# Kernel tuning notes

Hardware: AMD Instinct MI355X
Metric: run time of the kernel (lower is better)

## Reference

```python
import jax, jax.numpy as jnp
import numpy as np

FIR_LO = {
    'db4': np.array([-0.0105974017850021, 0.0328830116668852, 0.0308413818355607, -0.1870348117188811,
                     -0.0279837694169839, 0.6308807679295904, 0.7148465705529155, 0.2303778133088964], np.float32),
    'db6': np.array([0.00107730108499558, -0.00477725751101065, -0.0005538422009938, 0.03158203931748603,
                     0.02752286553030533, -0.0975016055873225, -0.12976686756709563, 0.22626469396544,
                     0.3152503517092432, -0.7511339080210959, 0.4946238903984534, 0.1115407433501095], np.float32),
    'sym6': np.array([-0.007800708325034148, 0.001767711864242804, 0.04472490177066578, -0.02106029251230056,
                      -0.0726375227866, 0.3379294217282401, 0.787641141030194, 0.4910559419267466,
                      -0.048311742585632, -0.1179901111484105, 0.00349071208421747, 0.01540410932702737], np.float32),
    'coif5': np.array([-3.459977283621256e-05, -7.098330313814114e-05, 0.0004662169601128863, 0.001117518770890601,
                       -0.002574517688750223, -0.00900797613666158, 0.015880544863615904, 0.03455502757306163,
                       -0.08230192710688598, -0.07179982161931202, 0.42848347637761874, 0.7937772226256206,
                       0.4051769024096169, -0.06112339000267287, -0.06577191128185562, 0.023452696141836267,
                       0.007782596427325418, -0.003793512864491014, -0.0002606761356811993, 0.000107502882505652,
                       1.10319778524429e-05, -5.520763127949e-06, -1.0682196848076e-06, 5.236425333584e-07,
                       1.125098976034e-07, -5.417490769329e-08, -8.8631e-09, 4.2921e-09, 6.7e-10, -3.2e-10], np.float32),
}

CANDIDATES = ['db4', 'db6', 'sym6', 'coif5', 'bior53', 'bior97']
LIFT_53 = [(-0.5, True), (0.25, False)]
LIFT_97 = [(-1.586134342, True), (-0.05298011854, False), (0.8829110762, True), (0.4435068522, False)]


def _pad_reflect(x, hpad, wpad):
    if hpad == (0, 0) and wpad == (0, 0):
        return x
    return jnp.pad(x, ((0, 0), (0, 0), hpad, wpad), mode='reflect')


def _lo(name):
    lo = jnp.asarray(FIR_LO[name])
    return lo / (jnp.sqrt(jnp.sum(lo * lo)) + 1e-12)


def _hi_from_lo(lo):
    L = lo.shape[0]
    sign = jnp.cos(jnp.pi * jnp.arange(L, dtype=lo.dtype))  # (-1)^n
    return sign * lo[::-1]


def _sep_conv(x, k, dim):
    # x: (N,1,H,W); k: (L,) 1D filter applied separably along dim (cross-correlation, stride 1)
    L = k.shape[0]
    pl = (L - 1) // 2
    pa, pb = ((pl - 1, pl) if L % 2 == 0 else (pl, pl))
    if dim == 'W':
        xp = _pad_reflect(x, (0, 0), (pa, pb))
        kern = k.reshape(1, 1, 1, L)
    else:
        xp = _pad_reflect(x, (pa, pb), (0, 0))
        kern = k.reshape(1, 1, L, 1)
    return jax.lax.conv_general_dilated(xp, kern, (1, 1), 'VALID',
                                        dimension_numbers=('NCHW', 'OIHW', 'NCHW'))


def _split_even_odd(x, dim):
    if dim == 'W':
        if x.shape[3] % 2 == 1:
            x = _pad_reflect(x, (0, 0), (0, 1))
        return x[..., 0::2], x[..., 1::2]
    if x.shape[2] % 2 == 1:
        x = _pad_reflect(x, (0, 1), (0, 0))
    return x[..., 0::2, :], x[..., 1::2, :]


def _nb_sum(x, dim):
    # 0.5*(left+right) with reflect padding == conv with kernel [0.5, 0, 0.5]
    if dim == 'W':
        xp = _pad_reflect(x, (0, 0), (1, 1))
        return 0.5 * (xp[..., :-2] + xp[..., 2:])
    xp = _pad_reflect(x, (1, 1), (0, 0))
    return 0.5 * (xp[..., :-2, :] + xp[..., 2:, :])


def _lift(x, dim, steps, sA, sD):
    even, odd = _split_even_odd(x, dim)
    for coeff, is_pred in steps:
        if is_pred:
            odd = odd + coeff * _nb_sum(even, dim)
        else:
            even = even + coeff * _nb_sum(odd, dim)
    return sA * even, sD * odd


def _one_level_1d(x, cand, dim, p):
    if cand == 'bior53':
        return _lift(x, dim, LIFT_53, p['s53A'], p['s53D'])
    if cand == 'bior97':
        return _lift(x, dim, LIFT_97, p['s97A'], p['s97D'])
    lo = _lo(cand)
    return _sep_conv(x, lo, dim), _sep_conv(x, _hi_from_lo(lo), dim)


def _one_level_2d(x, cand, p):
    H, W = x.shape[2], x.shape[3]
    Lw, Hw = _one_level_1d(x, cand, 'W', p)
    LL, LH = _one_level_1d(Lw, cand, 'H', p)
    HL, HH = _one_level_1d(Hw, cand, 'H', p)

    def up(t):
        if t.shape[2] == H and t.shape[3] == W:
            return t
        return jax.image.resize(t, (t.shape[0], t.shape[1], H, W), method='bilinear')  # align_corners=False

    hf = p['hf']
    return up(LL), up(LH) * hf, up(HL) * hf, up(HH) * hf


def reference(x, gate_w1, gate_b1, gate_w2, gate_b2, scale53_A, scale53_D,
              scale97_A, scale97_D, hf_scale, proj_w, proj_b):
    B, C, H, W = x.shape
    # gate: 1x1 conv -> relu -> 1x1 conv -> softmax over K candidates
    h = jax.nn.relu(jnp.einsum('bchw,oc->bohw', x, gate_w1) + gate_b1[None, :, None, None])
    logits = jnp.einsum('bchw,oc->bohw', h, gate_w2) + gate_b2[None, :, None, None]
    gate_w = jax.nn.softmax(logits, axis=1)  # (B,K,H,W)

    x_bc = x.reshape(B * C, 1, H, W)
    p = {'s53A': scale53_A, 's53D': scale53_D, 's97A': scale97_A, 's97D': scale97_D, 'hf': hf_scale}
    bands = [_one_level_2d(x_bc, c, p) for c in CANDIDATES]
    # stack over K candidates -> (B*C, K, H, W) per subband
    LL = jnp.concatenate([b[0] for b in bands], axis=1)
    LH = jnp.concatenate([b[1] for b in bands], axis=1)
    HL = jnp.concatenate([b[2] for b in bands], axis=1)
    HH = jnp.concatenate([b[3] for b in bands], axis=1)

    w = jnp.repeat(gate_w, C, axis=0)  # (B*C,K,H,W), same as repeat_interleave on batch
    w = w / (jnp.sum(w, axis=1, keepdims=True) + 1e-12)
    LL_f = jnp.sum(LL * w, axis=1)
    LH_f = jnp.sum(LH * w, axis=1)
    HL_f = jnp.sum(HL * w, axis=1)
    HH_f = jnp.sum(HH * w, axis=1)

    Y = jnp.stack([LL_f, LH_f, HL_f, HH_f], axis=1).reshape(B, C * 4, H, W)
    return jnp.einsum('bchw,oc->bohw', Y, proj_w) + proj_b[None, :, None, None]


def setup_inputs() -> dict:
    key = jax.random.key(0)
    ks = jax.random.split(key, 5)
    C, hidden, K, Cout = 32, 8, 6, 32
    return {
        'x': jax.random.normal(ks[0], (4, C, 192, 192), jnp.float32),
        'gate_w1': jax.random.normal(ks[1], (hidden, C), jnp.float32) * (1.0 / np.sqrt(C)),
        'gate_b1': jnp.zeros((hidden,), jnp.float32),
        'gate_w2': jax.random.normal(ks[2], (K, hidden), jnp.float32) * (1.0 / np.sqrt(hidden)),
        'gate_b2': jnp.zeros((K,), jnp.float32),
        'scale53_A': jnp.float32(1.0),
        'scale53_D': jnp.float32(1.0),
        'scale97_A': jnp.float32(1.149604398),
        'scale97_D': jnp.float32(1.0 / 1.149604398),
        'hf_scale': jnp.float32(0.9),
        'proj_w': jax.random.normal(ks[3], (Cout, 4 * C), jnp.float32) * (1.0 / np.sqrt(4 * C)),
        'proj_b': jnp.zeros((Cout,), jnp.float32),
    }
```

## Files before the change

kernel.cpp:

```cpp
#include <hip/hip_runtime.h>
#include <hip/hip_fp16.h>

#define HW 36864
#define IMGS 128

typedef _Float16 h16;
typedef _Float16 v8h __attribute__((ext_vector_type(8)));
typedef _Float16 v4h __attribute__((ext_vector_type(4)));
typedef _Float16 v2h __attribute__((ext_vector_type(2)));
typedef float v4f __attribute__((ext_vector_type(4)));

static __device__ __forceinline__ int imax(int a, int b) { return a > b ? a : b; }
static __device__ __forceinline__ int imin(int a, int b) { return a < b ? a : b; }

__device__ __constant__ float LIFT_C[6] = {
  -0.5f, 0.25f,
  -1.586134342f, -0.05298011854f, 0.8829110762f, 0.4435068522f
};
__device__ __constant__ int FIR_L[4]   = {8, 12, 12, 30};
__device__ __constant__ int FIR_PA[4]  = {2, 4, 4, 13};
__device__ __constant__ int FIR_OFF[4] = {0, 8, 20, 32};

__device__ constexpr float FIRC[62] = {
  -0.0105974017850021f, 0.0328830116668852f, 0.0308413818355607f, -0.1870348117188811f,
  -0.0279837694169839f, 0.6308807679295904f, 0.7148465705529155f, 0.2303778133088964f,
  0.00107730108499558f, -0.00477725751101065f, -0.0005538422009938f, 0.03158203931748603f,
  0.02752286553030533f, -0.0975016055873225f, -0.12976686756709563f, 0.22626469396544f,
  0.3152503517092432f, -0.7511339080210959f, 0.4946238903984534f, 0.1115407433501095f,
  -0.007800708325034148f, 0.001767711864242804f, 0.04472490177066578f, -0.02106029251230056f,
  -0.0726375227866f, 0.3379294217282401f, 0.787641141030194f, 0.4910559419267466f,
  -0.048311742585632f, -0.1179901111484105f, 0.00349071208421747f, 0.01540410932702737f,
  -3.459977283621256e-05f, -7.098330313814114e-05f, 0.0004662169601128863f, 0.001117518770890601f,
  -0.002574517688750223f, -0.00900797613666158f, 0.015880544863615904f, 0.03455502757306163f,
  -0.08230192710688598f, -0.07179982161931202f, 0.42848347637761874f, 0.7937772226256206f,
  0.4051769024096169f, -0.06112339000267287f, -0.06577191128185562f, 0.023452696141836267f,
  0.007782596427325418f, -0.003793512864491014f, -0.0002606761356811993f, 0.000107502882505652f,
  1.10319778524429e-05f, -5.520763127949e-06f, -1.0682196848076e-06f, 5.236425333584e-07f,
  1.125098976034e-07f, -5.417490769329e-08f, -8.8631e-09f, 4.2921e-09f, 6.7e-10f, -3.2e-10f,
};

__global__ __launch_bounds__(256) void k_gate(
    const float* __restrict__ x, const float* __restrict__ w1, const float* __restrict__ b1,
    const float* __restrict__ w2, const float* __restrict__ b2, h16* __restrict__ gate,
    h16* __restrict__ x16)
{
  __shared__ float w1s[256], b1s[8], w2s[48], b2s[6];
  int tid = threadIdx.x;
  w1s[tid] = w1[tid];
  if (tid < 8)  b1s[tid] = b1[tid];
  if (tid < 48) w2s[tid] = w2[tid];
  if (tid < 6)  b2s[tid] = b2[tid];
  __syncthreads();
  int px = blockIdx.x * 256 + tid;
  int b = px / HW, p = px - b * HW;
  const float* xb = x + (size_t)b * 32 * HW + p;
  h16* x16b = x16 + (size_t)b * 32 * HW + p;
  float xv[32];
#pragma unroll
  for (int c = 0; c < 32; ++c) xv[c] = xb[(size_t)c * HW];
#pragma unroll
  for (int c = 0; c < 32; ++c) x16b[(size_t)c * HW] = (h16)xv[c];
  float hb[8];
#pragma unroll
  for (int j = 0; j < 8; ++j) {
    float s = b1s[j];
#pragma unroll
    for (int c = 0; c < 32; ++c) s += w1s[j * 32 + c] * xv[c];
    hb[j] = fmaxf(s, 0.f);
  }
  float e[6], mx = -1e30f;
#pragma unroll
  for (int k = 0; k < 6; ++k) {
    float s = b2s[k];
#pragma unroll
    for (int j = 0; j < 8; ++j) s += w2s[k * 8 + j] * hb[j];
    e[k] = s; mx = fmaxf(mx, s);
  }
  float se = 0.f;
#pragma unroll
  for (int k = 0; k < 6; ++k) { e[k] = expf(e[k] - mx); se += e[k]; }
  float inv = 1.f / se, s2 = 0.f;
#pragma unroll
  for (int k = 0; k < 6; ++k) { e[k] *= inv; s2 += e[k]; }
  float inv2 = 1.f / (s2 + 1e-12f);
  h16* gp = gate + (size_t)b * 6 * HW + p;
#pragma unroll
  for (int k = 0; k < 6; ++k) gp[(size_t)k * HW] = (h16)(e[k] * inv2);
}

__global__ __launch_bounds__(64) void k_build(
    h16* __restrict__ Kall, const float* __restrict__ s53A, const float* __restrict__ s53D,
    const float* __restrict__ s97A, const float* __restrict__ s97D)
{
  const int col = blockIdx.x;
  const int mat = blockIdx.y;
  const int cand = mat >> 1, side = mat & 1;
  const int tid = threadIdx.x;
  h16* out = Kall + (size_t)mat * HW;
  if (cand < 4) {
    const int Lf = FIR_L[cand], PA = FIR_PA[cand], OFF = FIR_OFF[cand];
    float ss = 0.f;
    for (int j = 0; j < Lf; ++j) ss += FIRC[OFF + j] * FIRC[OFF + j];
    const float invn = 1.f / (sqrtf(ss) + 1e-12f);
    for (int i = tid; i < 192; i += 64) {
      const int d = (i < 96) ? 1 : 2;
      const int q0 = i - d;
      const int i0 = imax(q0, 0), i1 = imin(q0 + 1, 189);
      const float tt = (float)d - (float)(2 * i + 1) * (1.f / 192.f);
      float c0 = 0.f, c1 = 0.f;
      for (int j = 0; j < Lf; ++j) {
        float fj = side ? (((j & 1) ? -1.f : 1.f) * FIRC[OFF + Lf - 1 - j]) : FIRC[OFF + j];
        fj *= invn;
        int r0 = i0 + j - PA; r0 = r0 < 0 ? -r0 : (r0 > 191 ? 382 - r0 : r0);
        int r1 = i1 + j - PA; r1 = r1 < 0 ? -r1 : (r1 > 191 ? 382 - r1 : r1);
        if (r0 == col) c0 += fj;
        if (r1 == col) c1 += fj;
      }
      out[(size_t)i * 192 + col] = (h16)((1.f - tt) * c0 + tt * c1);
    }
  } else {
    __shared__ float yb[192];
    __shared__ float sb[96];
    yb[tid] = 0.f; yb[tid + 64] = 0.f; yb[tid + 128] = 0.f;
    __syncthreads();
    if (tid == 0) yb[col] = 1.f;
    __syncthreads();
    const int c97 = (cand == 5);
    const int base = c97 ? 2 : 0, ns = c97 ? 4 : 2;
    for (int s = 0; s < ns; ++s) {
      const float cf = LIFT_C[base + s] * 0.5f;
      for (int j = tid; j < 96; j += 64) {
        int jm = (j == 0) ? 1 : j - 1, jp = (j == 95) ? 94 : j + 1;
        if ((s & 1) == 0) yb[2 * j + 1] += cf * (yb[2 * jm] + yb[2 * jp]);
        else              yb[2 * j]     += cf * (yb[2 * jm + 1] + yb[2 * jp + 1]);
      }
      __syncthreads();
    }
    const float sA = c97 ? s97A[0] : s53A[0];
    const float sD = c97 ? s97D[0] : s53D[0];
    for (int u = tid; u < 96; u += 64)
      sb[u] = side ? sD * yb[2 * u + 1] : sA * yb[2 * u];
    __syncthreads();
    for (int i = tid; i < 192; i += 64) {
      const int u0 = (i >> 1) + (i & 1) - 1;
      const float tt = (i & 1) ? 0.25f : 0.75f;
      const int a0 = imax(u0, 0), a1 = imin(u0 + 1, 95);
      out[(size_t)i * 192 + col] = (h16)((1.f - tt) * sb[a0] + tt * sb[a1]);
    }
  }
}

__global__ __launch_bounds__(512, 2) void k_fuse(
    const h16* __restrict__ Kall, const h16* __restrict__ x16, const h16* __restrict__ gate,
    const float* __restrict__ hfp, h16* __restrict__ sf)
{
  __shared__ h16 Xs[192 * 136];
  __shared__ h16 Bs[48 * 200];
  const int bx = blockIdx.x;
  const int sw = bx & 1, qt = bx >> 1;
  const int img = blockIdx.y;
  const int bimg = img >> 5;
  const int tid = threadIdx.x;
  const int lane = tid & 63, wv = tid >> 6;
  const int lm = lane & 15, quad = lane >> 4;
  const int sh = wv & 1, w4 = wv >> 1;
  const int w0q = qt * 48;
  int ktb = (w0q - 24) >> 5; ktb = ktb < 0 ? 0 : (ktb > 2 ? 2 : ktb);

  const h16* xi = x16 + (size_t)img * HW + ktb * 32;
  for (int u = tid; u < 3072; u += 512) {
    int r = u >> 4, c8 = u & 15;
    *(v8h*)(Xs + r * 136 + c8 * 8) = *(const v8h*)(xi + (size_t)r * 192 + c8 * 8);
  }

  v4f acc[3][3];
#pragma unroll
  for (int mi = 0; mi < 3; ++mi)
#pragma unroll
    for (int nt = 0; nt < 3; ++nt) acc[mi][nt] = (v4f){0.f, 0.f, 0.f, 0.f};

  __syncthreads();

  for (int cand = 0; cand < 6; ++cand) {
    const h16* KW = Kall + (size_t)(cand * 2 + sw) * HW;
    for (int t = wv; t < 36; t += 8) {
      const int mi2 = t % 3, hj = t / 3;
      const int m0w = w0q + mi2 * 16;
      const int n0h = hj * 16;
      int ktr = (m0w - 24) >> 5; ktr = ktr < 0 ? 0 : (ktr > 3 ? 3 : ktr);
      v4f C = (v4f){0.f, 0.f, 0.f, 0.f};
#pragma unroll
      for (int kt = 0; kt < 3; ++kt) {
        const int s = ktr + kt;
        v8h aK = *(const v8h*)(KW + (size_t)(m0w + lm) * 192 + s * 32 + quad * 8);
        v8h bX = *(const v8h*)(Xs + (size_t)(n0h + lm) * 136 + (s - ktb) * 32 + quad * 8);
        C = __builtin_amdgcn_mfma_f32_16x16x32_f16(aK, bX, C, 0, 0, 0);
      }
#pragma unroll
      for (int r = 0; r < 4; ++r)
        Bs[(size_t)(mi2 * 16 + quad * 4 + r) * 200 + n0h + lm] = (h16)C[r];
    }
    __syncthreads();
    const h16* g16 = gate + (size_t)(bimg * 6 + cand) * HW;
    const h16* KB = Kall + (size_t)(cand * 2 + sh) * HW;
#pragma unroll
    for (int mi = 0; mi < 3; ++mi) {
      const int m0 = w4 * 48 + mi * 16;
      const int ktlo = imax(0, (m0 - 24) >> 5), kthi = imin(5, (m0 + 39) >> 5);
      const int hr0 = m0 + quad * 4;
      float g[3][4];
#pragma unroll
      for (int nt = 0; nt < 3; ++nt)
#pragma unroll
        for (int r = 0; r < 4; ++r)
          g[nt][r] = (float)g16[(size_t)(hr0 + r) * 192 + w0q + nt * 16 + lm];
      v4f C[3];
#pragma unroll
      for (int nt = 0; nt < 3; ++nt) C[nt] = (v4f){0.f, 0.f, 0.f, 0.f};
      for (int kt = ktlo; kt <= kthi; ++kt) {
        const int k0 = kt * 32 + quad * 8;
        v8h a = *(const v8h*)(KB + (size_t)(m0 + lm) * 192 + k0);
#pragma unroll
        for (int nt = 0; nt < 3; ++nt) {
          v8h b = *(const v8h*)(Bs + (size_t)(nt * 16 + lm) * 200 + k0);
          C[nt] = __builtin_amdgcn_mfma_f32_16x16x32_f16(a, b, C[nt], 0, 0, 0);
        }
      }
#pragma unroll
      for (int nt = 0; nt < 3; ++nt)
#pragma unroll
        for (int r = 0; r < 4; ++r)
          acc[mi][nt][r] += g[nt][r] * C[nt][r];
    }
    __syncthreads();
  }
  const float hfv = hfp[0];
  const int s = sw * 2 + sh;
  const float f = (s == 0) ? 1.f : hfv;
  h16* Op = sf + ((size_t)img * 4 + s) * HW;
#pragma unroll
  for (int mi = 0; mi < 3; ++mi) {
    const int hr0 = w4 * 48 + mi * 16 + quad * 4;
#pragma unroll
    for (int nt = 0; nt < 3; ++nt) {
      const int wc = w0q + nt * 16 + lm;
#pragma unroll
      for (int r = 0; r < 4; ++r)
        Op[(size_t)(hr0 + r) * 192 + wc] = (h16)(f * acc[mi][nt][r]);
    }
  }
}

__global__ __launch_bounds__(256) void k_proj(
    const h16* __restrict__ sf, const float* __restrict__ pw,
    const float* __restrict__ pb, float* __restrict__ out)
{
  const int tid = threadIdx.x;
  const int lane = tid & 63;
  const int og = __builtin_amdgcn_readfirstlane(tid >> 6);
  const int b = blockIdx.x / 288;
  const int p = (blockIdx.x - b * 288) * 128 + lane * 2;
  const h16* sfb = sf + (size_t)(b * 128) * HW + p;
  const float* pwb = pw + og * 8 * 128;
  float acc0[8], acc1[8];
#pragma unroll
  for (int oo = 0; oo < 8; ++oo) { acc0[oo] = 0.f; acc1[oo] = 0.f; }
#pragma unroll 4
  for (int ch = 0; ch < 128; ++ch) {
    v2h hv = *(const v2h*)(sfb + (size_t)ch * HW);
    const float v0 = (float)hv[0], v1 = (float)hv[1];
#pragma unroll
    for (int oo = 0; oo < 8; ++oo) {
      const float w = pwb[oo * 128 + ch];
      acc0[oo] = fmaf(w, v0, acc0[oo]);
      acc1[oo] = fmaf(w, v1, acc1[oo]);
    }
  }
#pragma unroll
  for (int oo = 0; oo < 8; ++oo) {
    float2 o2;
    o2.x = acc0[oo] + pb[og * 8 + oo];
    o2.y = acc1[oo] + pb[og * 8 + oo];
    *(float2*)(out + (size_t)(b * 32 + og * 8 + oo) * HW + p) = o2;
  }
}

extern "C" void kernel_launch(void* const* d_in, const int* in_sizes, int n_in,
                              void* d_out, int out_size, void* d_ws, size_t ws_size,
                              hipStream_t stream) {
  (void)in_sizes; (void)n_in; (void)out_size; (void)ws_size;
  const float* x    = (const float*)d_in[0];
  const float* gw1  = (const float*)d_in[1];
  const float* gb1  = (const float*)d_in[2];
  const float* gw2  = (const float*)d_in[3];
  const float* gb2  = (const float*)d_in[4];
  const float* s53A = (const float*)d_in[5];
  const float* s53D = (const float*)d_in[6];
  const float* s97A = (const float*)d_in[7];
  const float* s97D = (const float*)d_in[8];
  const float* hfp  = (const float*)d_in[9];
  const float* pw   = (const float*)d_in[10];
  const float* pb   = (const float*)d_in[11];
  float* out = (float*)d_out;

  h16* gate = (h16*)d_ws;
  h16* Kall = (h16*)((char*)d_ws + 1769472);
  h16* x16  = (h16*)((char*)d_ws + 2654208);
  h16* sf   = (h16*)((char*)d_ws + 40402944);

  hipLaunchKernelGGL(k_gate, dim3(576), dim3(256), 0, stream, x, gw1, gb1, gw2, gb2, gate, x16);
  hipLaunchKernelGGL(k_build, dim3(192, 12), dim3(64), 0, stream, Kall, s53A, s53D, s97A, s97D);
  hipLaunchKernelGGL(k_fuse, dim3(8, IMGS), dim3(512), 0, stream, Kall, x16, gate, hfp, sf);
  hipLaunchKernelGGL(k_proj, dim3(1152), dim3(256), 0, stream, sf, pw, pb, out);
}
```

Measured before the change: 307.8 us.

## Split k_fuse over output row bands to triple block count and shrink LDS

The fused wavelet kernel now splits each image tile into three output-row bands (hq), so the grid grows from 8 to 24 blocks per image. Each block loads only a 128-row window of the input into shared memory and computes a 48x128 intermediate instead of 48x192. Each wave handles one 16-row output tile instead of three. The smaller LDS footprint allows a launch bound of 3 blocks per CU. This raises occupancy and parallelism, but the first-stage row-filter products are recomputed across overlapping windows and there are more total block loads of the kernel matrices.

```diff
diff --git a/kernel.cpp b/kernel.cpp
--- a/kernel.cpp
+++ b/kernel.cpp
@@ -150,43 +150,46 @@
   }
 }
 
-__global__ __launch_bounds__(512, 2) void k_fuse(
+__global__ __launch_bounds__(512, 3) void k_fuse(
     const h16* __restrict__ Kall, const h16* __restrict__ x16, const h16* __restrict__ gate,
     const float* __restrict__ hfp, h16* __restrict__ sf)
 {
-  __shared__ h16 Xs[192 * 136];
-  __shared__ h16 Bs[48 * 200];
+  __shared__ h16 Xs[128 * 136];
+  __shared__ h16 Bs[48 * 136];
   const int bx = blockIdx.x;
-  const int sw = bx & 1, qt = bx >> 1;
+  const int sw = bx & 1, qt = (bx >> 1) & 3, hq = bx >> 3;
   const int img = blockIdx.y;
   const int bimg = img >> 5;
   const int tid = threadIdx.x;
   const int lane = tid & 63, wv = tid >> 6;
   const int lm = lane & 15, quad = lane >> 4;
-  const int sh = wv & 1, w4 = wv >> 1;
+  const int sh = wv & 1, mh = wv >> 1;
   const int w0q = qt * 48;
+  const int win0 = (hq == 0) ? 0 : (hq == 1 ? 40 : 64);
   int ktb = (w0q - 24) >> 5; ktb = ktb < 0 ? 0 : (ktb > 2 ? 2 : ktb);
 
-  const h16* xi = x16 + (size_t)img * HW + ktb * 32;
-  for (int u = tid; u < 3072; u += 512) {
+  const h16* xi = x16 + (size_t)img * HW + (size_t)win0 * 192 + ktb * 32;
+  for (int u = tid; u < 2048; u += 512) {
     int r = u >> 4, c8 = u & 15;
     *(v8h*)(Xs + r * 136 + c8 * 8) = *(const v8h*)(xi + (size_t)r * 192 + c8 * 8);
   }
 
-  v4f acc[3][3];
-#pragma unroll
-  for (int mi = 0; mi < 3; ++mi)
-#pragma unroll
-    for (int nt = 0; nt < 3; ++nt) acc[mi][nt] = (v4f){0.f, 0.f, 0.f, 0.f};
+  v4f acc[3];
+#pragma unroll
+  for (int nt = 0; nt < 3; ++nt) acc[nt] = (v4f){0.f, 0.f, 0.f, 0.f};
+
+  const int m0 = hq * 64 + mh * 16;
+  int kc0 = (m0 - 24 - win0) >> 5; kc0 = kc0 < 0 ? 0 : (kc0 > 1 ? 1 : kc0);
+  const int hr0 = m0 + quad * 4;
 
   __syncthreads();
 
   for (int cand = 0; cand < 6; ++cand) {
     const h16* KW = Kall + (size_t)(cand * 2 + sw) * HW;
-    for (int t = wv; t < 36; t += 8) {
-      const int mi2 = t % 3, hj = t / 3;
+    for (int t = wv; t < 24; t += 8) {
+      const int mi2 = t % 3, ht = t / 3;
       const int m0w = w0q + mi2 * 16;
-      const int n0h = hj * 16;
+      const int n0h = ht * 16;
       int ktr = (m0w - 24) >> 5; ktr = ktr < 0 ? 0 : (ktr > 3 ? 3 : ktr);
       v4f C = (v4f){0.f, 0.f, 0.f, 0.f};
 #pragma unroll
@@ -198,40 +201,35 @@
       }
 #pragma unroll
       for (int r = 0; r < 4; ++r)
-        Bs[(size_t)(mi2 * 16 + quad * 4 + r) * 200 + n0h + lm] = (h16)C[r];
+        Bs[(size_t)(mi2 * 16 + quad * 4 + r) * 136 + n0h + lm] = (h16)C[r];
     }
     __syncthreads();
     const h16* g16 = gate + (size_t)(bimg * 6 + cand) * HW;
     const h16* KB = Kall + (size_t)(cand * 2 + sh) * HW;
-#pragma unroll
-    for (int mi = 0; mi < 3; ++mi) {
-      const int m0 = w4 * 48 + mi * 16;
-      const int ktlo = imax(0, (m0 - 24) >> 5), kthi = imin(5, (m0 + 39) >> 5);
-      const int hr0 = m0 + quad * 4;
-      float g[3][4];
-#pragma unroll
-      for (int nt = 0; nt < 3; ++nt)
-#pragma unroll
-        for (int r = 0; r < 4; ++r)
-          g[nt][r] = (float)g16[(size_t)(hr0 + r) * 192 + w0q + nt * 16 + lm];
-      v4f C[3];
-#pragma unroll
-      for (int nt = 0; nt < 3; ++nt) C[nt] = (v4f){0.f, 0.f, 0.f, 0.f};
-      for (int kt = ktlo; kt <= kthi; ++kt) {
-        const int k0 = kt * 32 + quad * 8;
-        v8h a = *(const v8h*)(KB + (size_t)(m0 + lm) * 192 + k0);
-#pragma unroll
-        for (int nt = 0; nt < 3; ++nt) {
-          v8h b = *(const v8h*)(Bs + (size_t)(nt * 16 + lm) * 200 + k0);
-          C[nt] = __builtin_amdgcn_mfma_f32_16x16x32_f16(a, b, C[nt], 0, 0, 0);
-        }
+    float g[3][4];
+#pragma unroll
+    for (int nt = 0; nt < 3; ++nt)
+#pragma unroll
+      for (int r = 0; r < 4; ++r)
+        g[nt][r] = (float)g16[(size_t)(hr0 + r) * 192 + w0q + nt * 16 + lm];
+    v4f C[3];
+#pragma unroll
+    for (int nt = 0; nt < 3; ++nt) C[nt] = (v4f){0.f, 0.f, 0.f, 0.f};
+#pragma unroll
+    for (int kt = 0; kt < 3; ++kt) {
+      const int k0l = (kc0 + kt) * 32 + quad * 8;
+      v8h a = *(const v8h*)(KB + (size_t)(m0 + lm) * 192 + win0 + k0l);
+#pragma unroll
+      for (int nt = 0; nt < 3; ++nt) {
+        v8h b = *(const v8h*)(Bs + (size_t)(nt * 16 + lm) * 136 + k0l);
+        C[nt] = __builtin_amdgcn_mfma_f32_16x16x32_f16(a, b, C[nt], 0, 0, 0);
       }
-#pragma unroll
-      for (int nt = 0; nt < 3; ++nt)
-#pragma unroll
-        for (int r = 0; r < 4; ++r)
-          acc[mi][nt][r] += g[nt][r] * C[nt][r];
-    }
+    }
+#pragma unroll
+    for (int nt = 0; nt < 3; ++nt)
+#pragma unroll
+      for (int r = 0; r < 4; ++r)
+        acc[nt][r] += g[nt][r] * C[nt][r];
     __syncthreads();
   }
   const float hfv = hfp[0];
@@ -239,15 +237,11 @@
   const float f = (s == 0) ? 1.f : hfv;
   h16* Op = sf + ((size_t)img * 4 + s) * HW;
 #pragma unroll
-  for (int mi = 0; mi < 3; ++mi) {
-    const int hr0 = w4 * 48 + mi * 16 + quad * 4;
-#pragma unroll
-    for (int nt = 0; nt < 3; ++nt) {
-      const int wc = w0q + nt * 16 + lm;
-#pragma unroll
-      for (int r = 0; r < 4; ++r)
-        Op[(size_t)(hr0 + r) * 192 + wc] = (h16)(f * acc[mi][nt][r]);
-    }
+  for (int nt = 0; nt < 3; ++nt) {
+    const int wc = w0q + nt * 16 + lm;
+#pragma unroll
+    for (int r = 0; r < 4; ++r)
+      Op[(size_t)(hr0 + r) * 192 + wc] = (h16)(f * acc[nt][r]);
   }
 }
 
@@ -310,6 +304,6 @@
 
   hipLaunchKernelGGL(k_gate, dim3(576), dim3(256), 0, stream, x, gw1, gb1, gw2, gb2, gate, x16);
   hipLaunchKernelGGL(k_build, dim3(192, 12), dim3(64), 0, stream, Kall, s53A, s53D, s97A, s97D);
-  hipLaunchKernelGGL(k_fuse, dim3(8, IMGS), dim3(512), 0, stream, Kall, x16, gate, hfp, sf);
+  hipLaunchKernelGGL(k_fuse, dim3(24, IMGS), dim3(512), 0, stream, Kall, x16, gate, hfp, sf);
   hipLaunchKernelGGL(k_proj, dim3(1152), dim3(256), 0, stream, sf, pw, pb, out);
 }
```

After: 393.2 us. 1.28x slower.

## Split fused wavelet GEMM into separate width and height passes via global intermediate

Applied to the files above, without the earlier changes.

The fused kernel, which computed the width-direction transform into shared memory and then the height-direction transform, is split in two. A new k_gw kernel reads fp32 x directly, converts it to fp16 and writes all 12 plane products for every image to a large global buffer, PT. k_gh then reads PT instead of recomputing it per block. This removes the fp16 copy of x, the LDS staging and the per-block redundant width pass, at the cost of a roughly 113 MB intermediate written and read through global memory. The height pass now uses a fixed three-step k loop with banded operands held in registers.

```diff
diff --git a/kernel.cpp b/kernel.cpp
--- a/kernel.cpp
+++ b/kernel.cpp
@@ -6,7 +6,6 @@
 
 typedef _Float16 h16;
 typedef _Float16 v8h __attribute__((ext_vector_type(8)));
-typedef _Float16 v4h __attribute__((ext_vector_type(4)));
 typedef _Float16 v2h __attribute__((ext_vector_type(2)));
 typedef float v4f __attribute__((ext_vector_type(4)));
 
@@ -41,8 +40,7 @@
 
 __global__ __launch_bounds__(256) void k_gate(
     const float* __restrict__ x, const float* __restrict__ w1, const float* __restrict__ b1,
-    const float* __restrict__ w2, const float* __restrict__ b2, h16* __restrict__ gate,
-    h16* __restrict__ x16)
+    const float* __restrict__ w2, const float* __restrict__ b2, h16* __restrict__ gate)
 {
   __shared__ float w1s[256], b1s[8], w2s[48], b2s[6];
   int tid = threadIdx.x;
@@ -54,12 +52,9 @@
   int px = blockIdx.x * 256 + tid;
   int b = px / HW, p = px - b * HW;
   const float* xb = x + (size_t)b * 32 * HW + p;
-  h16* x16b = x16 + (size_t)b * 32 * HW + p;
   float xv[32];
 #pragma unroll
   for (int c = 0; c < 32; ++c) xv[c] = xb[(size_t)c * HW];
-#pragma unroll
-  for (int c = 0; c < 32; ++c) x16b[(size_t)c * HW] = (h16)xv[c];
   float hb[8];
 #pragma unroll
   for (int j = 0; j < 8; ++j) {
@@ -150,12 +145,58 @@
   }
 }
 
-__global__ __launch_bounds__(512, 2) void k_fuse(
-    const h16* __restrict__ Kall, const h16* __restrict__ x16, const h16* __restrict__ gate,
+__global__ __launch_bounds__(64) void k_gw(
+    const float* __restrict__ x, const h16* __restrict__ Kall, h16* __restrict__ PT)
+{
+  const int mt = blockIdx.x, img = blockIdx.y;
+  const int lane = threadIdx.x;
+  const int lm = lane & 15, quad = lane >> 4;
+  const int m0 = mt * 16;
+  int ktr = (m0 - 24) >> 5; ktr = ktr < 0 ? 0 : (ktr > 3 ? 3 : ktr);
+  const float* xi = x + (size_t)img * HW;
+  for (int hc = 0; hc < 3; ++hc) {
+    v8h b[4][3];
+#pragma unroll
+    for (int j = 0; j < 4; ++j)
+#pragma unroll
+      for (int kt = 0; kt < 3; ++kt) {
+        const float* xr = xi + (size_t)(hc * 64 + j * 16 + lm) * 192 + (ktr + kt) * 32 + quad * 8;
+        float4 u0 = *(const float4*)xr;
+        float4 u1 = *(const float4*)(xr + 4);
+        v8h t;
+        t[0] = (h16)u0.x; t[1] = (h16)u0.y; t[2] = (h16)u0.z; t[3] = (h16)u0.w;
+        t[4] = (h16)u1.x; t[5] = (h16)u1.y; t[6] = (h16)u1.z; t[7] = (h16)u1.w;
+        b[j][kt] = t;
+      }
+#pragma unroll 2
+    for (int plane = 0; plane < 12; ++plane) {
+      const h16* KW = Kall + (size_t)plane * HW + (size_t)(m0 + lm) * 192 + ktr * 32 + quad * 8;
+      v8h a0 = *(const v8h*)(KW);
+      v8h a1 = *(const v8h*)(KW + 32);
+      v8h a2 = *(const v8h*)(KW + 64);
+      v4f C[4];
+#pragma unroll
+      for (int j = 0; j < 4; ++j) C[j] = (v4f){0.f, 0.f, 0.f, 0.f};
+#pragma unroll
+      for (int j = 0; j < 4; ++j) {
+        C[j] = __builtin_amdgcn_mfma_f32_16x16x32_f16(a0, b[j][0], C[j], 0, 0, 0);
+        C[j] = __builtin_amdgcn_mfma_f32_16x16x32_f16(a1, b[j][1], C[j], 0, 0, 0);
+        C[j] = __builtin_amdgcn_mfma_f32_16x16x32_f16(a2, b[j][2], C[j], 0, 0, 0);
+      }
+      h16* Pp = PT + ((size_t)plane * IMGS + img) * HW;
+#pragma unroll
+      for (int j = 0; j < 4; ++j)
+#pragma unroll
+        for (int r = 0; r < 4; ++r)
+          Pp[(size_t)(m0 + quad * 4 + r) * 192 + hc * 64 + j * 16 + lm] = (h16)C[j][r];
+    }
+  }
+}
+
+__global__ __launch_bounds__(512, 2) void k_gh(
+    const h16* __restrict__ Kall, const h16* __restrict__ PT, const h16* __restrict__ gate,
     const float* __restrict__ hfp, h16* __restrict__ sf)
 {
-  __shared__ h16 Xs[192 * 136];
-  __shared__ h16 Bs[48 * 200];
   const int bx = blockIdx.x;
   const int sw = bx & 1, qt = bx >> 1;
   const int img = blockIdx.y;
@@ -165,13 +206,6 @@
   const int lm = lane & 15, quad = lane >> 4;
   const int sh = wv & 1, w4 = wv >> 1;
   const int w0q = qt * 48;
-  int ktb = (w0q - 24) >> 5; ktb = ktb < 0 ? 0 : (ktb > 2 ? 2 : ktb);
-
-  const h16* xi = x16 + (size_t)img * HW + ktb * 32;
-  for (int u = tid; u < 3072; u += 512) {
-    int r = u >> 4, c8 = u & 15;
-    *(v8h*)(Xs + r * 136 + c8 * 8) = *(const v8h*)(xi + (size_t)r * 192 + c8 * 8);
-  }
 
   v4f acc[3][3];
 #pragma unroll
@@ -179,34 +213,27 @@
 #pragma unroll
     for (int nt = 0; nt < 3; ++nt) acc[mi][nt] = (v4f){0.f, 0.f, 0.f, 0.f};
 
-  __syncthreads();
-
   for (int cand = 0; cand < 6; ++cand) {
-    const h16* KW = Kall + (size_t)(cand * 2 + sw) * HW;
-    for (int t = wv; t < 36; t += 8) {
-      const int mi2 = t % 3, hj = t / 3;
-      const int m0w = w0q + mi2 * 16;
-      const int n0h = hj * 16;
-      int ktr = (m0w - 24) >> 5; ktr = ktr < 0 ? 0 : (ktr > 3 ? 3 : ktr);
-      v4f C = (v4f){0.f, 0.f, 0.f, 0.f};
-#pragma unroll
-      for (int kt = 0; kt < 3; ++kt) {
-        const int s = ktr + kt;
-        v8h aK = *(const v8h*)(KW + (size_t)(m0w + lm) * 192 + s * 32 + quad * 8);
-        v8h bX = *(const v8h*)(Xs + (size_t)(n0h + lm) * 136 + (s - ktb) * 32 + quad * 8);
-        C = __builtin_amdgcn_mfma_f32_16x16x32_f16(aK, bX, C, 0, 0, 0);
-      }
-#pragma unroll
-      for (int r = 0; r < 4; ++r)
-        Bs[(size_t)(mi2 * 16 + quad * 4 + r) * 200 + n0h + lm] = (h16)C[r];
-    }
-    __syncthreads();
+    const h16* PB = PT + ((size_t)(cand * 2 + sw) * IMGS + img) * HW;
+    const h16* KB = Kall + (size_t)(cand * 2 + sh) * HW;
     const h16* g16 = gate + (size_t)(bimg * 6 + cand) * HW;
-    const h16* KB = Kall + (size_t)(cand * 2 + sh) * HW;
 #pragma unroll
     for (int mi = 0; mi < 3; ++mi) {
       const int m0 = w4 * 48 + mi * 16;
-      const int ktlo = imax(0, (m0 - 24) >> 5), kthi = imin(5, (m0 + 39) >> 5);
+      int ktr = (m0 - 24) >> 5; ktr = ktr < 0 ? 0 : (ktr > 3 ? 3 : ktr);
+      const int kb = ktr * 32 + quad * 8;
+      const h16* kr = KB + (size_t)(m0 + lm) * 192 + kb;
+      v8h a0 = *(const v8h*)(kr);
+      v8h a1 = *(const v8h*)(kr + 32);
+      v8h a2 = *(const v8h*)(kr + 64);
+      v8h b[3][3];
+#pragma unroll
+      for (int nt = 0; nt < 3; ++nt) {
+        const h16* pr = PB + (size_t)(w0q + nt * 16 + lm) * 192 + kb;
+        b[nt][0] = *(const v8h*)(pr);
+        b[nt][1] = *(const v8h*)(pr + 32);
+        b[nt][2] = *(const v8h*)(pr + 64);
+      }
       const int hr0 = m0 + quad * 4;
       float g[3][4];
 #pragma unroll
@@ -217,14 +244,11 @@
       v4f C[3];
 #pragma unroll
       for (int nt = 0; nt < 3; ++nt) C[nt] = (v4f){0.f, 0.f, 0.f, 0.f};
-      for (int kt = ktlo; kt <= kthi; ++kt) {
-        const int k0 = kt * 32 + quad * 8;
-        v8h a = *(const v8h*)(KB + (size_t)(m0 + lm) * 192 + k0);
-#pragma unroll
-        for (int nt = 0; nt < 3; ++nt) {
-          v8h b = *(const v8h*)(Bs + (size_t)(nt * 16 + lm) * 200 + k0);
-          C[nt] = __builtin_amdgcn_mfma_f32_16x16x32_f16(a, b, C[nt], 0, 0, 0);
-        }
+#pragma unroll
+      for (int nt = 0; nt < 3; ++nt) {
+        C[nt] = __builtin_amdgcn_mfma_f32_16x16x32_f16(a0, b[nt][0], C[nt], 0, 0, 0);
+        C[nt] = __builtin_amdgcn_mfma_f32_16x16x32_f16(a1, b[nt][1], C[nt], 0, 0, 0);
+        C[nt] = __builtin_amdgcn_mfma_f32_16x16x32_f16(a2, b[nt][2], C[nt], 0, 0, 0);
       }
 #pragma unroll
       for (int nt = 0; nt < 3; ++nt)
@@ -232,7 +256,6 @@
         for (int r = 0; r < 4; ++r)
           acc[mi][nt][r] += g[nt][r] * C[nt][r];
     }
-    __syncthreads();
   }
   const float hfv = hfp[0];
   const int s = sw * 2 + sh;
@@ -305,11 +328,12 @@
 
   h16* gate = (h16*)d_ws;
   h16* Kall = (h16*)((char*)d_ws + 1769472);
-  h16* x16  = (h16*)((char*)d_ws + 2654208);
-  h16* sf   = (h16*)((char*)d_ws + 40402944);
-
-  hipLaunchKernelGGL(k_gate, dim3(576), dim3(256), 0, stream, x, gw1, gb1, gw2, gb2, gate, x16);
+  h16* PT   = (h16*)((char*)d_ws + 2654208);
+  h16* sf   = (h16*)((char*)d_ws + 115900416);
+
+  hipLaunchKernelGGL(k_gate, dim3(576), dim3(256), 0, stream, x, gw1, gb1, gw2, gb2, gate);
   hipLaunchKernelGGL(k_build, dim3(192, 12), dim3(64), 0, stream, Kall, s53A, s53D, s97A, s97D);
-  hipLaunchKernelGGL(k_fuse, dim3(8, IMGS), dim3(512), 0, stream, Kall, x16, gate, hfp, sf);
+  hipLaunchKernelGGL(k_gw, dim3(12, IMGS), dim3(64), 0, stream, x, Kall, PT);
+  hipLaunchKernelGGL(k_gh, dim3(8, IMGS), dim3(512), 0, stream, Kall, PT, gate, hfp, sf);
   hipLaunchKernelGGL(k_proj, dim3(1152), dim3(256), 0, stream, sf, pw, pb, out);
 }
```

Result: slower. 394.4 us (+28.2%).
